# Optimization experiments

Measured on AMD Instinct MI355X. Metric: run time of the kernel, lower is better.

## Reference

```python
import jax, jax.numpy as jnp
import numpy as np

N = 20000   # nodes
E = 100000  # edges per relation
R = 4       # relations
H = 4       # heads
D = 64      # embed_dim (per-head dim == embed_dim in this module)
F = 128     # node_feat_dim
L = 2       # layers
EPS = 1e-5  # torch LayerNorm default


def setup_inputs() -> dict:
    key = jax.random.key(0)
    ks = jax.random.split(key, 32)
    s = 0.05
    inp = {}
    inp["nodes"] = jnp.arange(N)
    inp["node_features"] = jax.random.normal(ks[0], (N, F), jnp.float32)
    inp["betweenness"] = jax.random.uniform(ks[1], (N,), jnp.float32)
    inp["closeness"] = jax.random.uniform(ks[2], (N,), jnp.float32)
    inp["node_sign_influence"] = jax.random.normal(ks[3], (N,), jnp.float32)
    inp["edge_src"] = jax.random.randint(ks[4], (R, E), 0, N)
    inp["edge_tgt"] = jax.random.randint(ks[5], (R, E), 0, N)
    # encoder params
    inp["enc_Wf"] = jax.random.normal(ks[6], (F, D), jnp.float32) * s
    inp["enc_bf"] = jnp.full((D,), 0.01, jnp.float32)
    inp["enc_Wc"] = jax.random.normal(ks[7], (2, D), jnp.float32) * s
    inp["enc_bc"] = jnp.full((D,), 0.01, jnp.float32)
    # per-layer, per-relation attention params
    inp["Wq"] = jax.random.normal(ks[8], (L, R, D, D * H), jnp.float32) * s
    inp["bq"] = jnp.zeros((L, R, D * H), jnp.float32)
    inp["Wk"] = jax.random.normal(ks[9], (L, R, D, D * H), jnp.float32) * s
    inp["bk"] = jnp.zeros((L, R, D * H), jnp.float32)
    inp["Wv"] = jax.random.normal(ks[10], (L, R, D, D * H), jnp.float32) * s
    inp["bv"] = jnp.zeros((L, R, D * H), jnp.float32)
    inp["Wp"] = jax.random.normal(ks[11], (L, R * H * D, D), jnp.float32) * s
    inp["bp"] = jnp.zeros((L, D), jnp.float32)
    inp["sign_w"] = jax.random.normal(ks[12], (L, H, R), jnp.float32) * s
    inp["ln_g"] = jnp.ones((L, D), jnp.float32)
    inp["ln_b"] = jnp.zeros((L, D), jnp.float32)
    return inp


def reference(nodes, node_features, betweenness, closeness, node_sign_influence,
              edge_src, edge_tgt, enc_Wf, enc_bf, enc_Wc, enc_bc,
              Wq, bq, Wk, bk, Wv, bv, Wp, bp, sign_w, ln_g, ln_b):
    # CentralityAwareEncoder
    cen = jnp.stack([betweenness[nodes], closeness[nodes]], axis=1)  # [N, 2]
    x = node_features[nodes] @ enc_Wf + enc_bf + cen @ enc_Wc + enc_bc  # [N, D]
    n = x.shape[0]
    inv_sqrt_d = 1.0 / jnp.sqrt(jnp.float32(D))
    for l in range(L):  # structural loop over layers
        outs = []
        for r in range(R):  # structural loop over relations
            src, tgt = edge_src[r], edge_tgt[r]
            Q = (x @ Wq[l, r] + bq[l, r]).reshape(n, H, D)
            K = (x @ Wk[l, r] + bk[l, r]).reshape(n, H, D)
            V = (x @ Wv[l, r] + bv[l, r]).reshape(n, H, D)
            # edge-wise scores [E, H]
            scores = jnp.einsum('ehd,ehd->eh', Q[src], K[tgt]) * inv_sqrt_d
            scores = scores * (node_sign_influence[src][:, None] * sign_w[l, :, r][None, :])
            # segment softmax over src (all heads at once)
            mx = jax.ops.segment_max(scores, src, num_segments=n)
            ex = jnp.exp(scores - mx[src])
            den = jax.ops.segment_sum(ex, src, num_segments=n)
            attn = ex / (den[src] + 1e-10)  # [E, H]  (dropout: eval mode, identity)
            wV = V[tgt] * attn[..., None]   # [E, H, D]
            out = jax.ops.segment_sum(wV, src, num_segments=n)  # [N, H, D]
            outs.append(out.reshape(n, H * D))
        attn_out = jnp.concatenate(outs, axis=-1) @ Wp[l] + bp[l]  # [N, D]
        y = x + attn_out
        mu = y.mean(-1, keepdims=True)
        var = y.var(-1, keepdims=True)
        x = (y - mu) * jax.lax.rsqrt(var + EPS) * ln_g[l] + ln_b[l]
    return x
```

## Files before the change

kernel.cpp:

```cpp
#include <hip/hip_runtime.h>
#include <math.h>

#define NN 20000
#define EE 100000
#define RR 4
#define HH 4
#define DD 64
#define FF 128
#define LL 2

typedef __attribute__((ext_vector_type(8))) short bf16x8;
typedef __attribute__((ext_vector_type(4))) float f32x4;

__device__ __forceinline__ ushort f2bf(float f) {
  uint u = __float_as_uint(f);
  u += 0x7FFFu + ((u >> 16) & 1u);
  return (ushort)(u >> 16);
}
__device__ __forceinline__ float bf2f(ushort h) {
  return __uint_as_float((uint)h << 16);
}

__global__ __launch_bounds__(256) void enc_prep_kernel(
    const float* __restrict__ feat, const float* __restrict__ bet,
    const float* __restrict__ clo, const float* __restrict__ Wf,
    const float* __restrict__ bf, const float* __restrict__ Wc,
    const float* __restrict__ bc, float* __restrict__ x,
    ushort* __restrict__ xbf, const float* __restrict__ Wq,
    const float* __restrict__ bq, const float* __restrict__ Wk,
    const float* __restrict__ bk, const float* __restrict__ Wv,
    const float* __restrict__ bv, const float* __restrict__ Wp,
    ushort* __restrict__ mT, ushort* __restrict__ gT, float* __restrict__ cvec,
    float* __restrict__ gam) {
  const int t = threadIdx.x;
  if (blockIdx.x < 5000) {
    __shared__ float fs[4][FF];
    const int n0 = blockIdx.x * 4;
    for (int idx = t; idx < 4 * FF; idx += 256) {
      const int rr = idx >> 7, cc = idx & 127;
      const int n = n0 + rr;
      fs[rr][cc] = (n < NN) ? feat[(size_t)n * FF + cc] : 0.f;
    }
    __syncthreads();
    const int g = t >> 6, d = t & 63;
    const int n = n0 + g;
    if (n >= NN) return;
    float acc = bf[d] + bc[d] + bet[n] * Wc[d] + clo[n] * Wc[DD + d];
#pragma unroll 8
    for (int f = 0; f < FF; ++f) acc = fmaf(fs[g][f], Wf[f * DD + d], acc);
    x[(size_t)n * DD + d] = acc;
    xbf[(size_t)n * DD + d] = f2bf(acc);
    return;
  }
  const int idx = (blockIdx.x - 5000) * 256 + t;
  const int R1 = LL * RR * 272 * 64;
  const int R2 = LL * 64 * 1024;
  if (idx < R1) {
    const int lr = idx / (272 * 64);
    const int rem = idx % (272 * 64);
    const int col = rem >> 6, i = rem & 63;
    const float* wq = Wq + (size_t)lr * 64 * 256;
    const float* wk = Wk + (size_t)lr * 64 * 256;
    float v = 0.f;
    if (col < 256) {
      const int h = col >> 6, j = col & 63;
      const float* qa = wq + (size_t)i * 256 + h * 64;
      const float* kb = wk + (size_t)j * 256 + h * 64;
#pragma unroll 8
      for (int d = 0; d < 64; ++d) v = fmaf(qa[d], kb[d], v);
    } else if (col < 260) {
      const int h = col - 256;
      const float* qa = wq + (size_t)i * 256 + h * 64;
      const float* bb = bk + lr * 256 + h * 64;
#pragma unroll 8
      for (int d = 0; d < 64; ++d) v = fmaf(qa[d], bb[d], v);
    } else if (col < 264) {
      const int h = col - 260;
      const float* ka = wk + (size_t)i * 256 + h * 64;
      const float* bb = bq + lr * 256 + h * 64;
#pragma unroll 8
      for (int d = 0; d < 64; ++d) v = fmaf(ka[d], bb[d], v);
    }
    mT[idx] = f2bf(v);
  } else if (idx < R1 + R2) {
    const int id = idx - R1;
    const int lj = id >> 10;
    const int k = id & 1023;
    const int l = lj >> 6, j = lj & 63;
    const int r = k >> 8, h = (k >> 6) & 3, v_ = k & 63;
    const float* wv =
        Wv + (size_t)(l * RR + r) * 64 * 256 + (size_t)v_ * 256 + h * 64;
    const float* wp =
        Wp + (size_t)l * 65536 + (size_t)(r * 256 + h * 64) * 64 + j;
    float s = 0.f;
#pragma unroll 8
    for (int d = 0; d < 64; ++d) s = fmaf(wv[d], wp[d * 64], s);
    gT[id] = f2bf(s);
  } else if (idx < R1 + R2 + 512) {
    const int id = idx - R1 - R2;
    const int l = id >> 8, rj = id & 255;
    const int r = rj >> 6, j = rj & 63;
    const float* bb = bv + (l * RR + r) * 256;
    const float* wp = Wp + (size_t)l * 65536 + (size_t)(r * 256) * 64 + j;
    float s = 0.f;
    for (int q2 = 0; q2 < 256; ++q2) s = fmaf(bb[q2], wp[q2 * 64], s);
    cvec[id] = s;
  } else if (idx < R1 + R2 + 512 + 32) {
    const int id = idx - R1 - R2 - 512;
    const int lr = id >> 2, h = id & 3;
    const float* a = bq + lr * 256 + h * 64;
    const float* b2 = bk + lr * 256 + h * 64;
    float s = 0.f;
    for (int d = 0; d < 64; ++d) s = fmaf(a[d], b2[d], s);
    gam[id] = s;
  }
}

__global__ __launch_bounds__(256) void hist_kernel(
    const int* __restrict__ esrc, int* __restrict__ counts) {
  const int e = blockIdx.x * 256 + threadIdx.x;
  const int r = blockIdx.y;
  if (e < EE) atomicAdd(&counts[r * NN + esrc[(size_t)r * EE + e]], 1);
}

__global__ __launch_bounds__(1024) void scan_kernel(
    const int* __restrict__ counts, int* __restrict__ offs) {
  __shared__ int ts[1024];
  const int r = blockIdx.x, t = threadIdx.x;
  const int base = t * 20;
  int loc[20];
  int run = 0;
#pragma unroll
  for (int k = 0; k < 20; ++k) {
    const int i = base + k;
    const int v = (i < NN) ? counts[r * NN + i] : 0;
    run += v;
    loc[k] = run;
  }
  ts[t] = run;
  __syncthreads();
#pragma unroll
  for (int s = 1; s < 1024; s <<= 1) {
    const int add = (t >= s) ? ts[t - s] : 0;
    __syncthreads();
    ts[t] += add;
    __syncthreads();
  }
  const int prev = (t == 0) ? 0 : ts[t - 1];
#pragma unroll
  for (int k = 0; k < 20; ++k) {
    const int i = base + k;
    if (i < NN) offs[r * (NN + 1) + i + 1] = prev + loc[k];
  }
  if (t == 0) offs[r * (NN + 1)] = 0;
}

__global__ __launch_bounds__(256) void fill_kernel(
    const int* __restrict__ esrc, const int* __restrict__ etgt,
    const int* __restrict__ offs, int* __restrict__ cursor,
    int* __restrict__ csr) {
  const int e = blockIdx.x * 256 + threadIdx.x;
  const int r = blockIdx.y;
  if (e < EE) {
    const int s = esrc[(size_t)r * EE + e];
    const int pos = offs[r * (NN + 1) + s] + atomicAdd(&cursor[r * NN + s], 1);
    csr[(size_t)r * EE + pos] = etgt[(size_t)r * EE + e];
  }
}

__global__ __launch_bounds__(256) void yattn_kernel(
    const ushort* __restrict__ xbf, const int* __restrict__ offs4,
    const int* __restrict__ csr4, const float* __restrict__ nsi,
    const float* __restrict__ sw_l, const float* __restrict__ gam_l,
    const ushort* __restrict__ mT_l, ushort* __restrict__ attr) {
  __shared__ ushort ys[16][264];
  __shared__ float alph[16][4];
  const int t = threadIdx.x;
  const int w = t >> 6, l = t & 63;
  const int hi = l >> 4, lo = l & 15;
  const int h = hi;
  const int m0 = blockIdx.x * 16;
  const int r = blockIdx.y;
  const ushort* mTr = mT_l + (size_t)r * 17408;

  const ushort* arow = xbf + (size_t)(m0 + lo) * 64 + hi * 8;
  const bf16x8 a0 = *(const bf16x8*)(arow);
  const bf16x8 a1 = *(const bf16x8*)(arow + 32);
#pragma unroll
  for (int nt = 0; nt < 4; ++nt) {
    const int col0 = w * 64 + nt * 16;
    const ushort* brow = mTr + (size_t)(col0 + lo) * 64 + hi * 8;
    const bf16x8 b0 = *(const bf16x8*)(brow);
    const bf16x8 b1 = *(const bf16x8*)(brow + 32);
    f32x4 z = {0.f, 0.f, 0.f, 0.f};
    z = __builtin_amdgcn_mfma_f32_16x16x32_bf16(a0, b0, z, 0, 0, 0);
    z = __builtin_amdgcn_mfma_f32_16x16x32_bf16(a1, b1, z, 0, 0, 0);
    const int col = col0 + lo;
    const float wb = bf2f(mTr[(size_t)(260 + (col >> 6)) * 64 + (col & 63)]);
#pragma unroll
    for (int i = 0; i < 4; ++i) {
      ys[hi * 4 + i][col] = f2bf(z[i] + wb);
    }
  }
  if (w == 3) {
    const ushort* brow = mTr + (size_t)(256 + lo) * 64 + hi * 8;
    const bf16x8 b0 = *(const bf16x8*)(brow);
    const bf16x8 b1 = *(const bf16x8*)(brow + 32);
    f32x4 z = {0.f, 0.f, 0.f, 0.f};
    z = __builtin_amdgcn_mfma_f32_16x16x32_bf16(a0, b0, z, 0, 0, 0);
    z = __builtin_amdgcn_mfma_f32_16x16x32_bf16(a1, b1, z, 0, 0, 0);
    if (lo < 4) {
#pragma unroll
      for (int i = 0; i < 4; ++i) alph[hi * 4 + i][lo] = z[i];
    }
  }
  __syncthreads();

  const int* offs = offs4 + r * (NN + 1);
  const int* csr = csr4 + (size_t)r * EE;
  const float swh = sw_l[h * RR + r];
  const float gamh = gam_l[r * 4 + h];
#pragma unroll
  for (int k = 0; k < 4; ++k) {
    const int idx = w * 4 + k;
    const int n = m0 + idx;
    const ushort4 yu = *(const ushort4*)&ys[idx][l * 4];
    const float y0 = bf2f(yu.x), y1 = bf2f(yu.y), y2 = bf2f(yu.z),
                y3 = bf2f(yu.w);
    const float c2 = 0.18033688f * nsi[n] * swh;
    const float ac2 = (alph[idx][h] + gamh) * c2;
    const int s0 = offs[n], e0 = offs[n + 1];
    float denA = 0.f, oA0 = 0.f, oA1 = 0.f, oA2 = 0.f, oA3 = 0.f;
    float denB = 0.f, oB0 = 0.f, oB1 = 0.f, oB2 = 0.f, oB3 = 0.f;
    int i = s0;
    for (; i + 1 < e0; i += 2) {
      const int tgA = __builtin_amdgcn_readfirstlane(csr[i]);
      const int tgB = __builtin_amdgcn_readfirstlane(csr[i + 1]);
      const ushort4 cxA = *(const ushort4*)(xbf + (size_t)tgA * 64 + lo * 4);
      const ushort4 cxB = *(const ushort4*)(xbf + (size_t)tgB * 64 + lo * 4);
      const float xA0 = bf2f(cxA.x), xA1 = bf2f(cxA.y), xA2 = bf2f(cxA.z),
                  xA3 = bf2f(cxA.w);
      const float xB0 = bf2f(cxB.x), xB1 = bf2f(cxB.y), xB2 = bf2f(cxB.z),
                  xB3 = bf2f(cxB.w);
      float dA = y0 * xA0;
      float dB = y0 * xB0;
      dA = fmaf(y1, xA1, dA);
      dB = fmaf(y1, xB1, dB);
      dA = fmaf(y2, xA2, dA);
      dB = fmaf(y2, xB2, dB);
      dA = fmaf(y3, xA3, dA);
      dB = fmaf(y3, xB3, dB);
#pragma unroll
      for (int dd = 1; dd < 16; dd <<= 1) {
        dA += __shfl_xor(dA, dd);
        dB += __shfl_xor(dB, dd);
      }
      const float ewA = __builtin_amdgcn_exp2f(fmaf(dA, c2, ac2));
      const float ewB = __builtin_amdgcn_exp2f(fmaf(dB, c2, ac2));
      denA += ewA;
      denB += ewB;
      oA0 = fmaf(ewA, xA0, oA0);
      oB0 = fmaf(ewB, xB0, oB0);
      oA1 = fmaf(ewA, xA1, oA1);
      oB1 = fmaf(ewB, xB1, oB1);
      oA2 = fmaf(ewA, xA2, oA2);
      oB2 = fmaf(ewB, xB2, oB2);
      oA3 = fmaf(ewA, xA3, oA3);
      oB3 = fmaf(ewB, xB3, oB3);
    }
    if (i < e0) {
      const int tg = __builtin_amdgcn_readfirstlane(csr[i]);
      const ushort4 cx = *(const ushort4*)(xbf + (size_t)tg * 64 + lo * 4);
      const float x0 = bf2f(cx.x), x1 = bf2f(cx.y), x2 = bf2f(cx.z),
                  x3 = bf2f(cx.w);
      float d = y0 * x0;
      d = fmaf(y1, x1, d);
      d = fmaf(y2, x2, d);
      d = fmaf(y3, x3, d);
#pragma unroll
      for (int dd = 1; dd < 16; dd <<= 1) d += __shfl_xor(d, dd);
      const float ew = __builtin_amdgcn_exp2f(fmaf(d, c2, ac2));
      denA += ew;
      oA0 = fmaf(ew, x0, oA0);
      oA1 = fmaf(ew, x1, oA1);
      oA2 = fmaf(ew, x2, oA2);
      oA3 = fmaf(ew, x3, oA3);
    }
    const float inv = 1.f / (denA + denB + 1e-10f);
    ushort4 ou;
    ou.x = f2bf((oA0 + oB0) * inv);
    ou.y = f2bf((oA1 + oB1) * inv);
    ou.z = f2bf((oA2 + oB2) * inv);
    ou.w = f2bf((oA3 + oB3) * inv);
    *(ushort4*)(attr + (size_t)n * 1024 + r * 256 + l * 4) = ou;
  }
}

__global__ __launch_bounds__(256) void proj_ln_kernel(
    const ushort* __restrict__ attr, const ushort* __restrict__ gT,
    const float* __restrict__ xin, const float* __restrict__ bp,
    const float* __restrict__ g, const float* __restrict__ b,
    const int* __restrict__ offs4, const float* __restrict__ cvec_l,
    float* __restrict__ xout, ushort* __restrict__ xbf_out) {
  __shared__ float red[4][64][20];
  const int t = threadIdx.x;
  const int w = t >> 6, l = t & 63;
  const int hi = l >> 4, lo = l & 15;
  const int m0 = blockIdx.x * 16;
  const ushort* arow = attr + (size_t)(m0 + lo) * 1024 + w * 256 + hi * 8;
  f32x4 acc[4] = {{0.f, 0.f, 0.f, 0.f},
                  {0.f, 0.f, 0.f, 0.f},
                  {0.f, 0.f, 0.f, 0.f},
                  {0.f, 0.f, 0.f, 0.f}};
#pragma unroll
  for (int ks = 0; ks < 8; ++ks) {
    const bf16x8 a = *(const bf16x8*)(arow + ks * 32);
#pragma unroll
    for (int nt = 0; nt < 4; ++nt) {
      const bf16x8 bb = *(const bf16x8*)(gT + (size_t)(nt * 16 + lo) * 1024 +
                                         w * 256 + ks * 32 + hi * 8);
      acc[nt] = __builtin_amdgcn_mfma_f32_16x16x32_bf16(a, bb, acc[nt], 0, 0, 0);
    }
  }
#pragma unroll
  for (int nt = 0; nt < 4; ++nt) *(f32x4*)&red[w][l][nt * 4] = acc[nt];
  __syncthreads();
  if (w == 0) {
    f32x4 fin[4];
#pragma unroll
    for (int nt = 0; nt < 4; ++nt) {
      f32x4 s = *(const f32x4*)&red[0][l][nt * 4];
      s += *(const f32x4*)&red[1][l][nt * 4];
      s += *(const f32x4*)&red[2][l][nt * 4];
      s += *(const f32x4*)&red[3][l][nt * 4];
      fin[nt] = s;
    }
#pragma unroll
    for (int i = 0; i < 4; ++i) {
      const int gr = m0 + hi * 4 + i;
      float fl[4];
#pragma unroll
      for (int r = 0; r < 4; ++r) {
        fl[r] = (offs4[r * (NN + 1) + gr + 1] > offs4[r * (NN + 1) + gr])
                    ? 1.f
                    : 0.f;
      }
      float y[4];
      float s = 0.f, s2 = 0.f;
#pragma unroll
      for (int nt = 0; nt < 4; ++nt) {
        const int col = nt * 16 + lo;
        float extra = fl[0] * cvec_l[col] + fl[1] * cvec_l[64 + col] +
                      fl[2] * cvec_l[128 + col] + fl[3] * cvec_l[192 + col];
        const float yv =
            fin[nt][i] + bp[col] + extra + xin[(size_t)gr * 64 + col];
        y[nt] = yv;
        s += yv;
        s2 = fmaf(yv, yv, s2);
      }
#pragma unroll
      for (int d = 1; d < 16; d <<= 1) {
        s += __shfl_xor(s, d);
        s2 += __shfl_xor(s2, d);
      }
      const float mu = s * (1.f / 64.f);
      const float var = s2 * (1.f / 64.f) - mu * mu;
      const float rstd = rsqrtf(var + 1e-5f);
#pragma unroll
      for (int nt = 0; nt < 4; ++nt) {
        const int col = nt * 16 + lo;
        const float xo = (y[nt] - mu) * rstd * g[col] + b[col];
        xout[(size_t)gr * 64 + col] = xo;
        if (xbf_out) xbf_out[(size_t)gr * 64 + col] = f2bf(xo);
      }
    }
  }
}

extern "C" void kernel_launch(void* const* d_in, const int* in_sizes, int n_in,
                              void* d_out, int out_size, void* d_ws,
                              size_t ws_size, hipStream_t stream) {
  const float* feat = (const float*)d_in[1];
  const float* bet = (const float*)d_in[2];
  const float* clo = (const float*)d_in[3];
  const float* nsi = (const float*)d_in[4];
  const int* esrc = (const int*)d_in[5];
  const int* etgt = (const int*)d_in[6];
  const float* Wf = (const float*)d_in[7];
  const float* bf = (const float*)d_in[8];
  const float* Wc = (const float*)d_in[9];
  const float* bc = (const float*)d_in[10];
  const float* Wq = (const float*)d_in[11];
  const float* bq = (const float*)d_in[12];
  const float* Wk = (const float*)d_in[13];
  const float* bk = (const float*)d_in[14];
  const float* Wv = (const float*)d_in[15];
  const float* bv = (const float*)d_in[16];
  const float* Wp = (const float*)d_in[17];
  const float* bp = (const float*)d_in[18];
  const float* sw = (const float*)d_in[19];
  const float* lng = (const float*)d_in[20];
  const float* lnb = (const float*)d_in[21];
  float* out = (float*)d_out;

  char* base = (char*)d_ws;
  size_t off = 0;
  auto alloc = [&](size_t bytes) {
    void* p = base + off;
    off += (bytes + 255) & ~(size_t)255;
    return p;
  };
  float* xa = (float*)alloc((size_t)NN * DD * 4);
  float* xb = (float*)alloc((size_t)NN * DD * 4);
  ushort* xbf = (ushort*)alloc((size_t)NN * DD * 2);
  ushort* attr = (ushort*)alloc((size_t)NN * 1024 * 2);
  ushort* mT = (ushort*)alloc((size_t)LL * RR * 272 * 64 * 2);
  ushort* gT = (ushort*)alloc((size_t)LL * 64 * 1024 * 2);
  float* cvec = (float*)alloc((size_t)LL * RR * 64 * 4);
  float* gam = (float*)alloc((size_t)LL * RR * HH * 4);
  int* counts = (int*)alloc((size_t)RR * NN * 4);
  int* offsb = (int*)alloc((size_t)RR * (NN + 1) * 4);
  int* csr = (int*)alloc((size_t)RR * EE * 4);
  (void)ws_size;

  hipMemsetAsync(counts, 0, (size_t)RR * NN * 4, stream);
  {
    dim3 gg((EE + 255) / 256, RR);
    hipLaunchKernelGGL(hist_kernel, gg, dim3(256), 0, stream, esrc, counts);
  }
  hipLaunchKernelGGL(scan_kernel, dim3(RR), dim3(1024), 0, stream, counts,
                     offsb);
  hipMemsetAsync(counts, 0, (size_t)RR * NN * 4, stream);
  {
    dim3 gg((EE + 255) / 256, RR);
    hipLaunchKernelGGL(fill_kernel, gg, dim3(256), 0, stream, esrc, etgt, offsb,
                       counts, csr);
  }

  hipLaunchKernelGGL(enc_prep_kernel, dim3(6059), dim3(256), 0, stream, feat,
                     bet, clo, Wf, bf, Wc, bc, xa, xbf, Wq, bq, Wk, bk, Wv, bv,
                     Wp, mT, gT, cvec, gam);

  for (int l = 0; l < LL; ++l) {
    const float* xin = (l == 0) ? xa : xb;
    float* xout = (l == LL - 1) ? out : xb;
    ushort* xbf_next = (l == LL - 1) ? (ushort*)nullptr : xbf;
    hipLaunchKernelGGL(yattn_kernel, dim3(NN / 16, RR), dim3(256), 0, stream,
                       xbf, offsb, csr, nsi, sw + l * HH * RR, gam + l * 16,
                       mT + (size_t)l * RR * 17408, attr);
    hipLaunchKernelGGL(proj_ln_kernel, dim3(NN / 16), dim3(256), 0, stream,
                       attr, gT + (size_t)l * 65536, xin, bp + l * 64,
                       lng + l * 64, lnb + l * 64, offsb, cvec + l * 256, xout,
                       xbf_next);
  }
}
```

Baseline: 285.3 us.

## Fuse per-relation output projection into attention kernel, split LayerNorm into separate kernel

The attention kernel now runs 1024 threads per block, with one wave per node instead of four nodes per wave. After aggregation it applies the per-relation slice of the output projection directly from shared memory and writes fp32 per-relation partial projections. A new lightweight kernel sums the four partials, adds bias, residual and the empty-segment correction, then applies LayerNorm. This removes the bf16 attention buffer of width 1024 per node and the large projection reads, at the cost of writing and reading four fp32 partials per node, more work in each block, and an extra block-wide sync.

```diff
diff --git a/kernel.cpp b/kernel.cpp
--- a/kernel.cpp
+++ b/kernel.cpp
@@ -168,13 +168,15 @@
   }
 }
 
-__global__ __launch_bounds__(256) void yattn_kernel(
+__global__ __launch_bounds__(1024) void yattn_kernel(
     const ushort* __restrict__ xbf, const int* __restrict__ offs4,
     const int* __restrict__ csr4, const float* __restrict__ nsi,
     const float* __restrict__ sw_l, const float* __restrict__ gam_l,
-    const ushort* __restrict__ mT_l, ushort* __restrict__ attr) {
+    const ushort* __restrict__ mT_l, const ushort* __restrict__ gT,
+    float* __restrict__ partial) {
   __shared__ ushort ys[16][264];
   __shared__ float alph[16][4];
+  __shared__ float red[4][64][20];
   const int t = threadIdx.x;
   const int w = t >> 6, l = t & 63;
   const int hi = l >> 4, lo = l & 15;
@@ -186,9 +188,8 @@
   const ushort* arow = xbf + (size_t)(m0 + lo) * 64 + hi * 8;
   const bf16x8 a0 = *(const bf16x8*)(arow);
   const bf16x8 a1 = *(const bf16x8*)(arow + 32);
-#pragma unroll
-  for (int nt = 0; nt < 4; ++nt) {
-    const int col0 = w * 64 + nt * 16;
+  {
+    const int col0 = w * 16;
     const ushort* brow = mTr + (size_t)(col0 + lo) * 64 + hi * 8;
     const bf16x8 b0 = *(const bf16x8*)(brow);
     const bf16x8 b1 = *(const bf16x8*)(brow + 32);
@@ -202,7 +203,7 @@
       ys[hi * 4 + i][col] = f2bf(z[i] + wb);
     }
   }
-  if (w == 3) {
+  if (w == 0) {
     const ushort* brow = mTr + (size_t)(256 + lo) * 64 + hi * 8;
     const bf16x8 b0 = *(const bf16x8*)(brow);
     const bf16x8 b1 = *(const bf16x8*)(brow + 32);
@@ -216,19 +217,15 @@
   }
   __syncthreads();
 
-  const int* offs = offs4 + r * (NN + 1);
-  const int* csr = csr4 + (size_t)r * EE;
-  const float swh = sw_l[h * RR + r];
-  const float gamh = gam_l[r * 4 + h];
-#pragma unroll
-  for (int k = 0; k < 4; ++k) {
-    const int idx = w * 4 + k;
-    const int n = m0 + idx;
-    const ushort4 yu = *(const ushort4*)&ys[idx][l * 4];
+  {
+    const int n = m0 + w;
+    const int* offs = offs4 + r * (NN + 1);
+    const int* csr = csr4 + (size_t)r * EE;
+    const ushort4 yu = *(const ushort4*)&ys[w][l * 4];
     const float y0 = bf2f(yu.x), y1 = bf2f(yu.y), y2 = bf2f(yu.z),
                 y3 = bf2f(yu.w);
-    const float c2 = 0.18033688f * nsi[n] * swh;
-    const float ac2 = (alph[idx][h] + gamh) * c2;
+    const float c2 = 0.18033688f * nsi[n] * sw_l[h * RR + r];
+    const float ac2 = (alph[w][h] + gam_l[r * 4 + h]) * c2;
     const int s0 = offs[n], e0 = offs[n + 1];
     float denA = 0.f, oA0 = 0.f, oA1 = 0.f, oA2 = 0.f, oA3 = 0.f;
     float denB = 0.f, oB0 = 0.f, oB1 = 0.f, oB2 = 0.f, oB3 = 0.f;
@@ -292,38 +289,30 @@
     ou.y = f2bf((oA1 + oB1) * inv);
     ou.z = f2bf((oA2 + oB2) * inv);
     ou.w = f2bf((oA3 + oB3) * inv);
-    *(ushort4*)(attr + (size_t)n * 1024 + r * 256 + l * 4) = ou;
-  }
-}
-
-__global__ __launch_bounds__(256) void proj_ln_kernel(
-    const ushort* __restrict__ attr, const ushort* __restrict__ gT,
-    const float* __restrict__ xin, const float* __restrict__ bp,
-    const float* __restrict__ g, const float* __restrict__ b,
-    const int* __restrict__ offs4, const float* __restrict__ cvec_l,
-    float* __restrict__ xout, ushort* __restrict__ xbf_out) {
-  __shared__ float red[4][64][20];
-  const int t = threadIdx.x;
-  const int w = t >> 6, l = t & 63;
-  const int hi = l >> 4, lo = l & 15;
-  const int m0 = blockIdx.x * 16;
-  const ushort* arow = attr + (size_t)(m0 + lo) * 1024 + w * 256 + hi * 8;
-  f32x4 acc[4] = {{0.f, 0.f, 0.f, 0.f},
-                  {0.f, 0.f, 0.f, 0.f},
-                  {0.f, 0.f, 0.f, 0.f},
-                  {0.f, 0.f, 0.f, 0.f}};
-#pragma unroll
-  for (int ks = 0; ks < 8; ++ks) {
-    const bf16x8 a = *(const bf16x8*)(arow + ks * 32);
-#pragma unroll
-    for (int nt = 0; nt < 4; ++nt) {
-      const bf16x8 bb = *(const bf16x8*)(gT + (size_t)(nt * 16 + lo) * 1024 +
-                                         w * 256 + ks * 32 + hi * 8);
-      acc[nt] = __builtin_amdgcn_mfma_f32_16x16x32_bf16(a, bb, acc[nt], 0, 0, 0);
-    }
-  }
-#pragma unroll
-  for (int nt = 0; nt < 4; ++nt) *(f32x4*)&red[w][l][nt * 4] = acc[nt];
+    *(ushort4*)&ys[w][l * 4] = ou;
+  }
+  __syncthreads();
+
+  if (w < 4) {
+    f32x4 acc[4] = {{0.f, 0.f, 0.f, 0.f},
+                    {0.f, 0.f, 0.f, 0.f},
+                    {0.f, 0.f, 0.f, 0.f},
+                    {0.f, 0.f, 0.f, 0.f}};
+#pragma unroll
+    for (int ks = 0; ks < 2; ++ks) {
+      const bf16x8 a = *(const bf16x8*)&ys[lo][w * 64 + ks * 32 + hi * 8];
+#pragma unroll
+      for (int nt = 0; nt < 4; ++nt) {
+        const bf16x8 bb =
+            *(const bf16x8*)(gT + (size_t)(nt * 16 + lo) * 1024 + r * 256 +
+                             w * 64 + ks * 32 + hi * 8);
+        acc[nt] =
+            __builtin_amdgcn_mfma_f32_16x16x32_bf16(a, bb, acc[nt], 0, 0, 0);
+      }
+    }
+#pragma unroll
+    for (int nt = 0; nt < 4; ++nt) *(f32x4*)&red[w][l][nt * 4] = acc[nt];
+  }
   __syncthreads();
   if (w == 0) {
     f32x4 fin[4];
@@ -338,42 +327,47 @@
 #pragma unroll
     for (int i = 0; i < 4; ++i) {
       const int gr = m0 + hi * 4 + i;
-      float fl[4];
-#pragma unroll
-      for (int r = 0; r < 4; ++r) {
-        fl[r] = (offs4[r * (NN + 1) + gr + 1] > offs4[r * (NN + 1) + gr])
-                    ? 1.f
-                    : 0.f;
+#pragma unroll
+      for (int nt = 0; nt < 4; ++nt) {
+        partial[((size_t)r * NN + gr) * 64 + nt * 16 + lo] = fin[nt][i];
       }
-      float y[4];
-      float s = 0.f, s2 = 0.f;
-#pragma unroll
-      for (int nt = 0; nt < 4; ++nt) {
-        const int col = nt * 16 + lo;
-        float extra = fl[0] * cvec_l[col] + fl[1] * cvec_l[64 + col] +
-                      fl[2] * cvec_l[128 + col] + fl[3] * cvec_l[192 + col];
-        const float yv =
-            fin[nt][i] + bp[col] + extra + xin[(size_t)gr * 64 + col];
-        y[nt] = yv;
-        s += yv;
-        s2 = fmaf(yv, yv, s2);
-      }
-#pragma unroll
-      for (int d = 1; d < 16; d <<= 1) {
-        s += __shfl_xor(s, d);
-        s2 += __shfl_xor(s2, d);
-      }
-      const float mu = s * (1.f / 64.f);
-      const float var = s2 * (1.f / 64.f) - mu * mu;
-      const float rstd = rsqrtf(var + 1e-5f);
-#pragma unroll
-      for (int nt = 0; nt < 4; ++nt) {
-        const int col = nt * 16 + lo;
-        const float xo = (y[nt] - mu) * rstd * g[col] + b[col];
-        xout[(size_t)gr * 64 + col] = xo;
-        if (xbf_out) xbf_out[(size_t)gr * 64 + col] = f2bf(xo);
-      }
-    }
+    }
+  }
+}
+
+__global__ __launch_bounds__(256) void ln_kernel(
+    const float* __restrict__ partial, const float* __restrict__ xin,
+    const float* __restrict__ bp, const float* __restrict__ g,
+    const float* __restrict__ b, const int* __restrict__ offs4,
+    const float* __restrict__ cvec_l, float* __restrict__ xout,
+    ushort* __restrict__ xbf_out) {
+  const int t = threadIdx.x;
+  const int w = t >> 6, l = t & 63;
+  const int m0 = blockIdx.x * 16;
+#pragma unroll
+  for (int k = 0; k < 4; ++k) {
+    const int n = m0 + w * 4 + k;
+    float v = partial[((size_t)0 * NN + n) * 64 + l] +
+              partial[((size_t)1 * NN + n) * 64 + l] +
+              partial[((size_t)2 * NN + n) * 64 + l] +
+              partial[((size_t)3 * NN + n) * 64 + l];
+#pragma unroll
+    for (int r = 0; r < 4; ++r) {
+      const bool nz = offs4[r * (NN + 1) + n + 1] > offs4[r * (NN + 1) + n];
+      v += nz ? cvec_l[r * 64 + l] : 0.f;
+    }
+    const float y = v + bp[l] + xin[(size_t)n * 64 + l];
+    float s = y, s2 = y * y;
+#pragma unroll
+    for (int dd = 1; dd < 64; dd <<= 1) {
+      s += __shfl_xor(s, dd);
+      s2 += __shfl_xor(s2, dd);
+    }
+    const float mu = s * (1.f / 64.f);
+    const float var = s2 * (1.f / 64.f) - mu * mu;
+    const float xo = (y - mu) * rsqrtf(var + 1e-5f) * g[l] + b[l];
+    xout[(size_t)n * 64 + l] = xo;
+    if (xbf_out) xbf_out[(size_t)n * 64 + l] = f2bf(xo);
   }
 }
 
@@ -413,7 +407,7 @@
   float* xa = (float*)alloc((size_t)NN * DD * 4);
   float* xb = (float*)alloc((size_t)NN * DD * 4);
   ushort* xbf = (ushort*)alloc((size_t)NN * DD * 2);
-  ushort* attr = (ushort*)alloc((size_t)NN * 1024 * 2);
+  float* partial = (float*)alloc((size_t)RR * NN * 64 * 4);
   ushort* mT = (ushort*)alloc((size_t)LL * RR * 272 * 64 * 2);
   ushort* gT = (ushort*)alloc((size_t)LL * 64 * 1024 * 2);
   float* cvec = (float*)alloc((size_t)LL * RR * 64 * 4);
@@ -445,12 +439,12 @@
     const float* xin = (l == 0) ? xa : xb;
     float* xout = (l == LL - 1) ? out : xb;
     ushort* xbf_next = (l == LL - 1) ? (ushort*)nullptr : xbf;
-    hipLaunchKernelGGL(yattn_kernel, dim3(NN / 16, RR), dim3(256), 0, stream,
+    hipLaunchKernelGGL(yattn_kernel, dim3(NN / 16, RR), dim3(1024), 0, stream,
                        xbf, offsb, csr, nsi, sw + l * HH * RR, gam + l * 16,
-                       mT + (size_t)l * RR * 17408, attr);
-    hipLaunchKernelGGL(proj_ln_kernel, dim3(NN / 16), dim3(256), 0, stream,
-                       attr, gT + (size_t)l * 65536, xin, bp + l * 64,
-                       lng + l * 64, lnb + l * 64, offsb, cvec + l * 256, xout,
-                       xbf_next);
-  }
-}
+                       mT + (size_t)l * RR * 17408, gT + (size_t)l * 65536,
+                       partial);
+    hipLaunchKernelGGL(ln_kernel, dim3(NN / 16), dim3(256), 0, stream, partial,
+                       xin, bp + l * 64, lng + l * 64, lnb + l * 64, offsb,
+                       cvec + l * 256, xout, xbf_next);
+  }
+}
```

Measured after the change: 329.8 us. 15.6% more time.
